# Kernel optimization log

Hardware: AMD Instinct MI355X
Metric: run time of the kernel (lower is better)

The kernel has to match this reference:

```python
import jax, jax.numpy as jnp
import numpy as np
import math

DIM = 1024
N_HEADS = 16
HEAD_DIM = DIM // N_HEADS
FFN_HIDDEN = 4096
EPS = 1e-6


def setup_inputs() -> dict:
    key = jax.random.key(0)
    ks = jax.random.split(key, 10)
    s = 1.0 / math.sqrt(DIM)
    sh = 1.0 / math.sqrt(FFN_HIDDEN)
    return {
        "x": jax.random.normal(ks[0], (2, 2048, DIM), dtype=jnp.float32),
        # attention weights stored as [in, out] (y = x @ W)
        "wq": jax.random.normal(ks[1], (DIM, DIM), dtype=jnp.float32) * s,
        "wk": jax.random.normal(ks[2], (DIM, DIM), dtype=jnp.float32) * s,
        "wv": jax.random.normal(ks[3], (DIM, DIM), dtype=jnp.float32) * s,
        "wo": jax.random.normal(ks[4], (DIM, DIM), dtype=jnp.float32) * s,
        "w_gate": jax.random.normal(ks[5], (DIM, FFN_HIDDEN), dtype=jnp.float32) * s,
        "w_up": jax.random.normal(ks[6], (DIM, FFN_HIDDEN), dtype=jnp.float32) * s,
        "w_down": jax.random.normal(ks[7], (FFN_HIDDEN, DIM), dtype=jnp.float32) * sh,
        "attn_norm_w": jnp.ones((DIM,), dtype=jnp.float32),
        "ffn_norm_w": jnp.ones((DIM,), dtype=jnp.float32),
    }


def rmsnorm(x, w):
    xf = x.astype(jnp.float32)
    rms = jax.lax.rsqrt(jnp.mean(xf * xf, axis=-1, keepdims=True) + EPS)
    return (xf * rms).astype(x.dtype) * w


def attention(x, wq, wk, wv, wo):
    B, T, C = x.shape
    q = (x @ wq).reshape(B, T, N_HEADS, HEAD_DIM)
    k = (x @ wk).reshape(B, T, N_HEADS, HEAD_DIM)
    v = (x @ wv).reshape(B, T, N_HEADS, HEAD_DIM)
    scores = jnp.einsum("bqhd,bkhd->bhqk", q, k) / math.sqrt(HEAD_DIM)
    causal = jnp.tril(jnp.ones((T, T), dtype=bool))  # True = keep
    scores = jnp.where(causal, scores, -jnp.inf)
    attn = jax.nn.softmax(scores, axis=-1)
    out = jnp.einsum("bhqk,bkhd->bqhd", attn, v).reshape(B, T, C)
    return out @ wo


def swiglu(x, w_gate, w_up, w_down):
    return (jax.nn.silu(x @ w_gate) * (x @ w_up)) @ w_down


def reference(x, wq, wk, wv, wo, w_gate, w_up, w_down, attn_norm_w, ffn_norm_w):
    x = x + attention(rmsnorm(x, attn_norm_w), wq, wk, wv, wo)
    x = x + swiglu(rmsnorm(x, ffn_norm_w), w_gate, w_up, w_down)
    return x
```

## Files before the change

kernel.cpp:

```cpp
#include <hip/hip_runtime.h>
#include <hip/hip_bf16.h>
#include <stdint.h>
#include <math.h>

#define DIM   1024
#define TSEQ  2048
#define BATCH 2
#define NH    16
#define HD    64
#define FFN   4096
#define ROWS  (BATCH*TSEQ)
#define QKVN  (3*DIM)

typedef __attribute__((ext_vector_type(8))) short s16x8;
typedef __attribute__((ext_vector_type(4))) float f32x4;

__device__ __forceinline__ unsigned short f2bf(float f) {
  union { float f; unsigned u; } v; v.f = f;
  unsigned r = v.u + 0x7fffu + ((v.u >> 16) & 1u);
  return (unsigned short)(r >> 16);
}
__device__ __forceinline__ float bf2f(unsigned short h) {
  union { unsigned u; float f; } v; v.u = ((unsigned)h) << 16; return v.f;
}
__device__ __forceinline__ unsigned pack_bf2(float lo, float hi) {
  union { float f; unsigned u; } a, c; a.f = lo; c.f = hi;
  return (c.u & 0xffff0000u) | (a.u >> 16);
}

__device__ __forceinline__ void gld16(const void* g, void* l) {
  __builtin_amdgcn_global_load_lds((const __attribute__((address_space(1))) void*)g,
                                   (__attribute__((address_space(3))) void*)l, 16, 0, 0);
}

__device__ __forceinline__ int xcd_swz_flat() {
  const int nx = gridDim.x, ny = gridDim.y;
  const int nwg = nx * ny * gridDim.z;
  const int flat = blockIdx.x + nx * (blockIdx.y + ny * blockIdx.z);
  return (flat & 7) * (nwg >> 3) + (flat >> 3);
}

__global__ void wtrans_k(const float* __restrict__ w, unsigned short* __restrict__ wt,
                         int K, int N, int mode)
{
  __shared__ unsigned short t[64][65];
  const int n0 = blockIdx.x * 64, k0 = blockIdx.y * 64;
  const int tid = threadIdx.x;
  #pragma unroll
  for (int i = 0; i < 16; ++i) {
    const int r = i*4 + (tid >> 6), c = tid & 63;
    t[r][c] = f2bf(w[(size_t)(k0 + r) * N + n0 + c]);
  }
  __syncthreads();
  #pragma unroll
  for (int i = 0; i < 16; ++i) {
    const int r = i*4 + (tid >> 6), c = tid & 63;
    const int n = n0 + r;
    int dr = n;
    if (mode == 1) dr = ((n >> 4) << 5) + (n & 15);
    if (mode == 2) dr = ((n >> 4) << 5) + 16 + (n & 15);
    wt[(size_t)dr * K + k0 + c] = t[c][r];
  }
}

__global__ void wtrans_qkv_k(const float* __restrict__ wq, const float* __restrict__ wk,
                             const float* __restrict__ wv, unsigned short* __restrict__ wt)
{
  __shared__ unsigned short t[64][65];
  const int n0 = blockIdx.x * 64, k0 = blockIdx.y * 64, z = blockIdx.z;
  const float* w = (z == 0) ? wq : (z == 1) ? wk : wv;
  unsigned short* dst = wt + (size_t)z * DIM * DIM;
  const int tid = threadIdx.x;
  #pragma unroll
  for (int i = 0; i < 16; ++i) {
    const int r = i*4 + (tid >> 6), c = tid & 63;
    t[r][c] = f2bf(w[(size_t)(k0 + r) * DIM + n0 + c]);
  }
  __syncthreads();
  #pragma unroll
  for (int i = 0; i < 16; ++i) {
    const int r = i*4 + (tid >> 6), c = tid & 63;
    dst[(size_t)(n0 + r) * DIM + k0 + c] = t[c][r];
  }
}

__global__ void vtrans_k(const unsigned short* __restrict__ qkv, unsigned short* __restrict__ vt)
{
  __shared__ unsigned short t[64][65];
  const int tt0 = blockIdx.x * 64;
  const int bh = blockIdx.y, b = bh >> 4, h = bh & 15;
  const int tid = threadIdx.x;
  const unsigned short* src = qkv + (size_t)(b*TSEQ + tt0) * QKVN + 2*DIM + h*HD;
  #pragma unroll
  for (int i = 0; i < 16; ++i) {
    const int r = i*4 + (tid >> 6), c = tid & 63;
    t[r][c] = src[(size_t)r * QKVN + c];
  }
  __syncthreads();
  unsigned short* dst = vt + (size_t)bh * HD * TSEQ + tt0;
  #pragma unroll
  for (int i = 0; i < 16; ++i) {
    const int d = i*4 + (tid >> 6), c = tid & 63;
    dst[(size_t)d * TSEQ + c] = t[c][d];
  }
}

__global__ void rmsnorm_k(const float* __restrict__ x, const float* __restrict__ w,
                          unsigned short* __restrict__ o)
{
  const int row = blockIdx.x, tid = threadIdx.x;
  const float4 v = ((const float4*)(x + (size_t)row * DIM))[tid];
  float ss = v.x*v.x + v.y*v.y + v.z*v.z + v.w*v.w;
  #pragma unroll
  for (int off = 32; off >= 1; off >>= 1) ss += __shfl_xor(ss, off);
  __shared__ float sred[4];
  if ((tid & 63) == 0) sred[tid >> 6] = ss;
  __syncthreads();
  const float tot = sred[0] + sred[1] + sred[2] + sred[3];
  const float r = rsqrtf(tot * (1.0f/DIM) + 1e-6f);
  const float4 wv = ((const float4*)w)[tid];
  ushort4 ov;
  ov.x = f2bf(v.x*r*wv.x); ov.y = f2bf(v.y*r*wv.y);
  ov.z = f2bf(v.z*r*wv.z); ov.w = f2bf(v.w*r*wv.w);
  ((ushort4*)(o + (size_t)row * DIM))[tid] = ov;
}

__global__ void rmsnorm3_k(const float* __restrict__ x, const float* __restrict__ p0,
                           const float* __restrict__ p1, const float* __restrict__ w,
                           float* __restrict__ x1, unsigned short* __restrict__ o)
{
  const int row = blockIdx.x, tid = threadIdx.x;
  const size_t base = (size_t)row * DIM;
  const float4 a = ((const float4*)(x + base))[tid];
  const float4 b = ((const float4*)(p0 + base))[tid];
  const float4 c = ((const float4*)(p1 + base))[tid];
  float4 v;
  v.x = a.x + b.x + c.x; v.y = a.y + b.y + c.y;
  v.z = a.z + b.z + c.z; v.w = a.w + b.w + c.w;
  ((float4*)(x1 + base))[tid] = v;
  float ss = v.x*v.x + v.y*v.y + v.z*v.z + v.w*v.w;
  #pragma unroll
  for (int off = 32; off >= 1; off >>= 1) ss += __shfl_xor(ss, off);
  __shared__ float sred[4];
  if ((tid & 63) == 0) sred[tid >> 6] = ss;
  __syncthreads();
  const float tot = sred[0] + sred[1] + sred[2] + sred[3];
  const float r = rsqrtf(tot * (1.0f/DIM) + 1e-6f);
  const float4 wv = ((const float4*)w)[tid];
  ushort4 ov;
  ov.x = f2bf(v.x*r*wv.x); ov.y = f2bf(v.y*r*wv.y);
  ov.z = f2bf(v.z*r*wv.z); ov.w = f2bf(v.w*r*wv.w);
  ((ushort4*)(o + base))[tid] = ov;
}

__global__ void resadd3_k(const float* __restrict__ x1, const float* __restrict__ q0,
                          const float* __restrict__ q1, float* __restrict__ o)
{
  const size_t i = (size_t)blockIdx.x * 256 + threadIdx.x;
  const float4 a = ((const float4*)x1)[i];
  const float4 b = ((const float4*)q0)[i];
  const float4 c = ((const float4*)q1)[i];
  float4 v;
  v.x = a.x + b.x + c.x; v.y = a.y + b.y + c.y;
  v.z = a.z + b.z + c.z; v.w = a.w + b.w + c.w;
  ((float4*)o)[i] = v;
}

__global__ void gemm128sp(const unsigned short* __restrict__ A, int lda,
                          const unsigned short* __restrict__ BT, int ldb,
                          float* __restrict__ P, int ldc, int Khalf)
{
  __shared__ __align__(16) unsigned short lA[128*64];
  __shared__ __align__(16) unsigned short lB[128*64];
  const int nx = gridDim.x, ny = gridDim.y;
  const int w = xcd_swz_flat();
  const int bx = w % nx, by = (w / nx) % ny, bz = w / (nx * ny);
  const int tid = threadIdx.x;
  const int lane = tid & 63;
  const int wid = tid >> 6;
  const int m0 = by * 128, n0 = bx * 128;
  const int Koff = bz * Khalf;
  P += (size_t)bz * ((size_t)ny * 128) * ldc;
  const int wr = (wid >> 1) * 64, wc = (wid & 1) * 64;
  const int lrow = lane & 15, lk8 = (lane >> 4) * 8;

  f32x4 acc[4][4] = {};

  for (int k0 = Koff; k0 < Koff + Khalf; k0 += 64) {
    #pragma unroll
    for (int c = 0; c < 4; ++c) {
      const int boff = c*4096 + tid*16;
      const int row = boff >> 7, colb = boff & 127;
      gld16((const char*)A + ((size_t)(m0+row)*lda + k0)*2 + colb, (char*)lA + boff);
    }
    #pragma unroll
    for (int c = 0; c < 4; ++c) {
      const int boff = c*4096 + tid*16;
      const int row = boff >> 7, colb = boff & 127;
      gld16((const char*)BT + ((size_t)(n0+row)*ldb + k0)*2 + colb, (char*)lB + boff);
    }
    __syncthreads();
    #pragma unroll
    for (int kk = 0; kk < 64; kk += 32) {
      s16x8 af[4], bf[4];
      #pragma unroll
      for (int i = 0; i < 4; ++i) af[i] = *(const s16x8*)&lA[(wr + i*16 + lrow)*64 + kk + lk8];
      #pragma unroll
      for (int j = 0; j < 4; ++j) bf[j] = *(const s16x8*)&lB[(wc + j*16 + lrow)*64 + kk + lk8];
      #pragma unroll
      for (int i = 0; i < 4; ++i)
        #pragma unroll
        for (int j = 0; j < 4; ++j)
          acc[i][j] = __builtin_amdgcn_mfma_f32_16x16x32_bf16(af[i], bf[j], acc[i][j], 0, 0, 0);
    }
    __syncthreads();
  }
  const int er = (lane >> 4) * 4, ec = lane & 15;
  #pragma unroll
  for (int i = 0; i < 4; ++i)
    #pragma unroll
    for (int j = 0; j < 4; ++j) {
      const int gr = m0 + wr + i*16 + er;
      const int gc = n0 + wc + j*16 + ec;
      #pragma unroll
      for (int e = 0; e < 4; ++e)
        P[(size_t)(gr + e) * ldc + gc] = acc[i][j][e];
    }
}

template<int EPI>
__global__ __launch_bounds__(512) void gemm256(const unsigned short* __restrict__ A, int lda,
                                               const unsigned short* __restrict__ BT, int ldb,
                                               void* __restrict__ Cout, int ldc, int K)
{
  __shared__ __align__(16) unsigned short lA[2][256*64];
  __shared__ __align__(16) unsigned short lB[2][256*64];
  const int nx = gridDim.x;
  const int wsz = xcd_swz_flat();
  const int bx = wsz % nx, by = wsz / nx;
  const int tid = threadIdx.x, lane = tid & 63, wid = tid >> 6;
  const int lrow = lane & 15, g = lane >> 4;
  const int wm = wid >> 2, wn = wid & 3;
  const int m0 = by * 256, n0 = bx * 256;

  const int r0 = tid >> 3;
  const int eB = ((r0 >> 5) << 6) | (r0 & 31);
  const int lc0 = ((tid & 7) * 16) ^ ((r0 & 7) << 4);
  const char* pA = (const char*)A + ((size_t)(m0 + r0) * lda) * 2 + lc0;
  const char* pB = (const char*)BT + ((size_t)(n0 + eB) * ldb) * 2 + lc0;
  char* dA = (char*)&lA[0][0] + tid * 16;
  char* dB = (char*)&lB[0][0] + eB * 128 + (tid & 7) * 16;
  const size_t a64 = (size_t)64 * lda * 2;
  const size_t b32 = (size_t)32 * ldb * 2;

#define STG_GA0(t) do { const char* s_ = pA + (size_t)(t) * 128; \
    char* d_ = dA + (((t) & 1) * 32768); \
    gld16(s_, d_); gld16(s_ + 2*a64, d_ + 16384); } while (0)
#define STG_GA1(t) do { const char* s_ = pA + (size_t)(t) * 128 + a64; \
    char* d_ = dA + (((t) & 1) * 32768) + 8192; \
    gld16(s_, d_); gld16(s_ + 2*a64, d_ + 16384); } while (0)
#define STG_GB0(t) do { const char* s_ = pB + (size_t)(t) * 128; \
    char* d_ = dB + (((t) & 1) * 32768); \
    gld16(s_, d_); gld16(s_ + 4*b32, d_ + 16384); } while (0)
#define STG_GB1(t) do { const char* s_ = pB + (size_t)(t) * 128 + b32; \
    char* d_ = dB + (((t) & 1) * 32768) + 4096; \
    gld16(s_, d_); gld16(s_ + 4*b32, d_ + 16384); } while (0)

  const int swz = (lrow & 7) << 4;
  const int c0 = (g * 16) ^ swz;
  const int c1 = c0 ^ 64;
  const char* rdA = (const char*)&lA[0][0] + (wm * 128 + lrow) * 128;
  const char* rdB = (const char*)&lB[0][0] + (wn * 64 + lrow) * 128;

  f32x4 acc[8][4] = {};
  s16x8 a0[4][2], a1[4][2], b0[2][2], b1[2][2];

#define MFMA_Q(rh, ch, AF, BF) do { \
    _Pragma("unroll") \
    for (int i_ = 0; i_ < 4; ++i_) { \
      _Pragma("unroll") \
      for (int j_ = 0; j_ < 2; ++j_) { \
        acc[(rh)*4+i_][(ch)*2+j_] = __builtin_amdgcn_mfma_f32_16x16x32_bf16(AF[i_][0], BF[j_][0], acc[(rh)*4+i_][(ch)*2+j_], 0,0,0); \
        acc[(rh)*4+i_][(ch)*2+j_] = __builtin_amdgcn_mfma_f32_16x16x32_bf16(AF[i_][1], BF[j_][1], acc[(rh)*4+i_][(ch)*2+j_], 0,0,0); \
      } } } while (0)

#define VMCNT(n) asm volatile("s_waitcnt vmcnt(" #n ")" ::: "memory")
#define LGKM0()  do { asm volatile("s_waitcnt lgkmcnt(0)" ::: "memory"); \
                      __builtin_amdgcn_sched_barrier(0); } while (0)
#define BARRIER() do { __builtin_amdgcn_s_barrier(); \
                       __builtin_amdgcn_sched_barrier(0); } while (0)

#define DS_A0(buf) do { _Pragma("unroll") for (int i_ = 0; i_ < 4; ++i_) { \
    a0[i_][0] = *(const s16x8*)((buf) + i_*2048 + c0); \
    a0[i_][1] = *(const s16x8*)((buf) + i_*2048 + c1); } } while (0)
#define DS_A1(buf) do { _Pragma("unroll") for (int i_ = 0; i_ < 4; ++i_) { \
    a1[i_][0] = *(const s16x8*)((buf) + 8192 + i_*2048 + c0); \
    a1[i_][1] = *(const s16x8*)((buf) + 8192 + i_*2048 + c1); } } while (0)
#define DS_B0(buf) do { _Pragma("unroll") for (int j_ = 0; j_ < 2; ++j_) { \
    b0[j_][0] = *(const s16x8*)((buf) + j_*2048 + c0); \
    b0[j_][1] = *(const s16x8*)((buf) + j_*2048 + c1); } } while (0)
#define DS_B1(buf) do { _Pragma("unroll") for (int j_ = 0; j_ < 2; ++j_) { \
    b1[j_][0] = *(const s16x8*)((buf) + 4096 + j_*2048 + c0); \
    b1[j_][1] = *(const s16x8*)((buf) + 4096 + j_*2048 + c1); } } while (0)

#define PRIO_MFMA(rh, ch, AF, BF) do { \
    __builtin_amdgcn_s_setprio(1); MFMA_Q(rh, ch, AF, BF); \
    __builtin_amdgcn_s_setprio(0); } while (0)

  const int NT = K >> 6;

  STG_GA0(0); STG_GB0(0); STG_GB1(0); STG_GA1(0);
  VMCNT(4);
  BARRIER();

  for (int t = 0; t < NT - 1; ++t) {
    const char* bufA = rdA + (t & 1) * 32768;
    const char* bufB = rdB + (t & 1) * 32768;
    STG_GA0(t + 1); STG_GB0(t + 1);
    DS_A0(bufA); DS_B0(bufB);
    LGKM0();
    PRIO_MFMA(0, 0, a0, b0);
    VMCNT(6); BARRIER();
    STG_GB1(t + 1);
    DS_B1(bufB);
    LGKM0();
    PRIO_MFMA(0, 1, a0, b1);
    VMCNT(6); BARRIER();
    STG_GA1(t + 1);
    DS_A1(bufA);
    LGKM0();
    PRIO_MFMA(1, 1, a1, b1);
    BARRIER();
    PRIO_MFMA(1, 0, a1, b0);
    VMCNT(4); BARRIER();
  }
  {
    const char* bufA = rdA + ((NT - 1) & 1) * 32768;
    const char* bufB = rdB + ((NT - 1) & 1) * 32768;
    DS_A0(bufA); DS_B0(bufB);
    LGKM0();
    PRIO_MFMA(0, 0, a0, b0);
    VMCNT(2); BARRIER();
    DS_B1(bufB);
    LGKM0();
    PRIO_MFMA(0, 1, a0, b1);
    VMCNT(0); BARRIER();
    DS_A1(bufA);
    LGKM0();
    PRIO_MFMA(1, 1, a1, b1);
    PRIO_MFMA(1, 0, a1, b0);
  }

  const int er = g * 4, ec = lane & 15;
  if (EPI == 0) {
    unsigned short* C = (unsigned short*)Cout;
    #pragma unroll
    for (int i = 0; i < 8; ++i)
      #pragma unroll
      for (int j = 0; j < 4; ++j) {
        const int gr = m0 + wm*128 + i*16 + er;
        const int gc = n0 + wn*64 + j*16 + ec;
        #pragma unroll
        for (int e = 0; e < 4; ++e)
          C[(size_t)(gr + e) * ldc + gc] = f2bf(acc[i][j][e]);
      }
  } else {
    unsigned short* C = (unsigned short*)Cout;
    #pragma unroll
    for (int i = 0; i < 8; ++i)
      #pragma unroll
      for (int tp = 0; tp < 2; ++tp) {
        const int gr = m0 + wm*128 + i*16 + er;
        const int hc = (n0 >> 1) + wn*32 + tp*16 + ec;
        #pragma unroll
        for (int e = 0; e < 4; ++e) {
          const float gv = acc[i][2*tp][e];
          const float uv = acc[i][2*tp + 1][e];
          const float hv = gv / (1.f + __expf(-gv)) * uv;
          C[(size_t)(gr + e) * ldc + hc] = f2bf(hv);
        }
      }
  }
#undef STG_GA0
#undef STG_GA1
#undef STG_GB0
#undef STG_GB1
#undef MFMA_Q
#undef VMCNT
#undef LGKM0
#undef BARRIER
#undef DS_A0
#undef DS_A1
#undef DS_B0
#undef DS_B1
#undef PRIO_MFMA
}

__global__ __launch_bounds__(512) void attn_fwd(const unsigned short* __restrict__ qkv,
                                                const unsigned short* __restrict__ vt,
                                                unsigned short* __restrict__ outp)
{
  __shared__ __align__(16) unsigned short lK[2][64*64];
  __shared__ __align__(16) unsigned short lV[2][64*64];
  const int nx = gridDim.x;
  const int wsz = xcd_swz_flat();
  const int qblk = wsz % nx;
  const int bh = wsz / nx, b = bh >> 4, h = bh & 15;
  const int tid = threadIdx.x, wid = tid >> 6, lane = tid & 63;
  const int lq = lane & 15, g = lane >> 4;

  const int qrow = qblk*128 + wid*16;
  const int myq = qrow + lq;

  const size_t qbase = ((size_t)(b*TSEQ + myq)) * QKVN + h*HD;
  const s16x8 qf0 = *(const s16x8*)&qkv[qbase + g*8];
  const s16x8 qf1 = *(const s16x8*)&qkv[qbase + 32 + g*8];

  const int boff = tid * 16;
  const int loff = boff ^ (((boff >> 7) & 7) << 4);
  const int srow = loff >> 7;
  const int scolb = loff & 127;
  const char* ksrc0 = (const char*)qkv +
      (((size_t)(b*TSEQ + srow)) * QKVN + DIM + h*HD) * 2 + scolb;
  const char* vsrc0 = (const char*)vt +
      (((size_t)bh*HD + srow) * TSEQ) * 2 + scolb;

  float mrun = -INFINITY, lrun = 0.f;
  f32x4 of[4] = {};

  const int nkt = 2*qblk + 2;

  gld16(ksrc0, (char*)lK[0] + boff);
  gld16(vsrc0, (char*)lV[0] + boff);
  int cur = 0;

  for (int kt = 0; kt < nkt; ++kt) {
    __syncthreads();
    if (kt + 1 < nkt) {
      gld16(ksrc0 + (size_t)(kt+1)*64*(QKVN*2), (char*)lK[cur^1] + boff);
      gld16(vsrc0 + (size_t)(kt+1)*128,         (char*)lV[cur^1] + boff);
    }
    if (kt*64 <= qrow + 15) {
      const unsigned short* Kb = lK[cur];
      const unsigned short* Vb = lV[cur];
      f32x4 sacc[4] = {};
      #pragma unroll
      for (int s = 0; s < 4; ++s) {
        const int r = s*16 + lq;
        const int sw = (r & 7) << 4;
        const s16x8 kf0 = *(const s16x8*)((const char*)Kb + r*128 + ((g*16) ^ sw));
        const s16x8 kf1 = *(const s16x8*)((const char*)Kb + r*128 + ((64 + g*16) ^ sw));
        sacc[s] = __builtin_amdgcn_mfma_f32_16x16x32_bf16(kf0, qf0, sacc[s], 0,0,0);
        sacc[s] = __builtin_amdgcn_mfma_f32_16x16x32_bf16(kf1, qf1, sacc[s], 0,0,0);
      }
      float p[4][4];
      float mt = -INFINITY;
      #pragma unroll
      for (int s = 0; s < 4; ++s)
        #pragma unroll
        for (int e = 0; e < 4; ++e) {
          const int key = kt*64 + s*16 + 4*g + e;
          const float v = (key <= myq) ? sacc[s][e]*0.125f : -INFINITY;
          p[s][e] = v;
          mt = fmaxf(mt, v);
        }
      mt = fmaxf(mt, __shfl_xor(mt, 16));
      mt = fmaxf(mt, __shfl_xor(mt, 32));
      const float mnew = fmaxf(mrun, mt);
      const float scale = __expf(mrun - mnew);
      float ssum = 0.f;
      #pragma unroll
      for (int s = 0; s < 4; ++s)
        #pragma unroll
        for (int e = 0; e < 4; ++e) {
          p[s][e] = __expf(p[s][e] - mnew);
          ssum += p[s][e];
        }
      ssum += __shfl_xor(ssum, 16);
      ssum += __shfl_xor(ssum, 32);
      lrun = lrun * scale + ssum;
      mrun = mnew;
      #pragma unroll
      for (int d0b = 0; d0b < 4; ++d0b) of[d0b] = of[d0b] * scale;
      #pragma unroll
      for (int hh = 0; hh < 2; ++hh) {
        unsigned w[4];
        #pragma unroll
        for (int j = 0; j < 4; ++j) w[j] = pack_bf2(p[2*hh][j], p[2*hh+1][j]);
        s16x8 bp;
        #pragma unroll
        for (int e = 0; e < 8; ++e) {
          const int srcg = 2*(g & 1) + (e >> 2);
          const unsigned ww = (unsigned)__shfl((int)w[e & 3], lq | (srcg << 4));
          bp[e] = (short)((g >= 2) ? (ww >> 16) : (ww & 0xffffu));
        }
        #pragma unroll
        for (int d0b = 0; d0b < 4; ++d0b) {
          const int r = d0b*16 + lq;
          const int sw = (r & 7) << 4;
          const s16x8 vf = *(const s16x8*)((const char*)Vb + r*128 + ((hh*64 + g*16) ^ sw));
          of[d0b] = __builtin_amdgcn_mfma_f32_16x16x32_bf16(vf, bp, of[d0b], 0,0,0);
        }
      }
    }
    cur ^= 1;
  }
  const float inv = 1.f / lrun;
  const size_t obase = ((size_t)(b*TSEQ + myq)) * DIM + h*HD;
  #pragma unroll
  for (int d0b = 0; d0b < 4; ++d0b) {
    ushort4 o;
    o.x = f2bf(of[d0b][0] * inv);
    o.y = f2bf(of[d0b][1] * inv);
    o.z = f2bf(of[d0b][2] * inv);
    o.w = f2bf(of[d0b][3] * inv);
    *(ushort4*)&outp[obase + d0b*16 + 4*g] = o;
  }
}

extern "C" void kernel_launch(void* const* d_in, const int* in_sizes, int n_in,
                              void* d_out, int out_size, void* d_ws, size_t ws_size,
                              hipStream_t stream)
{
  const float* x   = (const float*)d_in[0];
  const float* wq  = (const float*)d_in[1];
  const float* wk  = (const float*)d_in[2];
  const float* wv  = (const float*)d_in[3];
  const float* wo  = (const float*)d_in[4];
  const float* wg  = (const float*)d_in[5];
  const float* wu  = (const float*)d_in[6];
  const float* wd  = (const float*)d_in[7];
  const float* anw = (const float*)d_in[8];
  const float* fnw = (const float*)d_in[9];
  float* outp = (float*)d_out;

  const size_t MB = 1024*1024;
  char* ws = (char*)d_ws;
  float*          x1    = (float*)         (ws + 0);
  unsigned short* wdT   = (unsigned short*)(ws + 16*MB);
  unsigned short* wguT  = (unsigned short*)(ws + 24*MB);
  unsigned short* wqkvT = (unsigned short*)(ws + 40*MB);
  unsigned short* woT   = (unsigned short*)(ws + 46*MB);
  unsigned short* xn    = (unsigned short*)(ws + 48*MB);
  unsigned short* qkv   = (unsigned short*)(ws + 56*MB);
  unsigned short* vtb   = (unsigned short*)(ws + 80*MB);
  unsigned short* aout  = (unsigned short*)(ws + 88*MB);
  float*          pwo   = (float*)         (ws + 56*MB);
  unsigned short* hbuf  = (unsigned short*)(ws + 56*MB);
  float*          pdn   = (float*)         (ws + 24*MB);

  const dim3 blk(256);

  wtrans_qkv_k<<<dim3(16,16,3), blk, 0, stream>>>(wq, wk, wv, wqkvT);
  wtrans_k<<<dim3(16,16), blk, 0, stream>>>(wo, woT, DIM, DIM, 0);
  wtrans_k<<<dim3(64,16), blk, 0, stream>>>(wg, wguT, DIM, FFN, 1);
  wtrans_k<<<dim3(64,16), blk, 0, stream>>>(wu, wguT, DIM, FFN, 2);
  wtrans_k<<<dim3(16,64), blk, 0, stream>>>(wd, wdT, FFN, DIM, 0);

  rmsnorm_k<<<ROWS, blk, 0, stream>>>(x, anw, xn);
  gemm256<0><<<dim3(QKVN/256, ROWS/256), dim3(512), 0, stream>>>(xn, DIM, wqkvT, DIM, qkv, QKVN, DIM);
  vtrans_k<<<dim3(TSEQ/64, BATCH*NH), blk, 0, stream>>>(qkv, vtb);
  attn_fwd<<<dim3(TSEQ/128, BATCH*NH), dim3(512), 0, stream>>>(qkv, vtb, aout);
  gemm128sp<<<dim3(DIM/128, ROWS/128, 2), blk, 0, stream>>>(aout, DIM, woT, DIM, pwo, DIM, DIM/2);
  rmsnorm3_k<<<ROWS, blk, 0, stream>>>(x, pwo, pwo + (size_t)ROWS*DIM, fnw, x1, xn);

  gemm256<2><<<dim3(2*FFN/256, ROWS/256), dim3(512), 0, stream>>>(xn, DIM, wguT, DIM, hbuf, FFN, DIM);
  gemm128sp<<<dim3(DIM/128, ROWS/128, 2), blk, 0, stream>>>(hbuf, FFN, wdT, FFN, pdn, DIM, FFN/2);
  resadd3_k<<<dim3(ROWS*DIM/1024), blk, 0, stream>>>(x1, pdn, pdn + (size_t)ROWS*DIM, outp);
}
```

Before: 347.6 us.

## Deepen gemm256 prefetch pipeline, XCD-tiled block mapping, bf16 split-K partials, 4-way down-proj split

Restructures the gemm256 main loop so global loads for the next tile are issued earlier, with register reads for the next stage overlapping the current MFMA quarter. It also replaces the generic XCD swizzle with a CX×CY region mapping meant to improve L2 locality per XCD. Split-K partials in gemm128sp are now stored as bf16 instead of fp32, which halves partial traffic at some cost in precision. The down projection is split 4 ways to raise parallelism, with a 5-input residual add to combine the partials.

```diff
diff --git a/kernel.cpp b/kernel.cpp
--- a/kernel.cpp
+++ b/kernel.cpp
@@ -125,18 +125,18 @@
   ((ushort4*)(o + (size_t)row * DIM))[tid] = ov;
 }
 
-__global__ void rmsnorm3_k(const float* __restrict__ x, const float* __restrict__ p0,
-                           const float* __restrict__ p1, const float* __restrict__ w,
+__global__ void rmsnorm3_k(const float* __restrict__ x, const unsigned short* __restrict__ p0,
+                           const unsigned short* __restrict__ p1, const float* __restrict__ w,
                            float* __restrict__ x1, unsigned short* __restrict__ o)
 {
   const int row = blockIdx.x, tid = threadIdx.x;
   const size_t base = (size_t)row * DIM;
   const float4 a = ((const float4*)(x + base))[tid];
-  const float4 b = ((const float4*)(p0 + base))[tid];
-  const float4 c = ((const float4*)(p1 + base))[tid];
+  const ushort4 b = ((const ushort4*)(p0 + base))[tid];
+  const ushort4 c = ((const ushort4*)(p1 + base))[tid];
   float4 v;
-  v.x = a.x + b.x + c.x; v.y = a.y + b.y + c.y;
-  v.z = a.z + b.z + c.z; v.w = a.w + b.w + c.w;
+  v.x = a.x + bf2f(b.x) + bf2f(c.x); v.y = a.y + bf2f(b.y) + bf2f(c.y);
+  v.z = a.z + bf2f(b.z) + bf2f(c.z); v.w = a.w + bf2f(b.w) + bf2f(c.w);
   ((float4*)(x1 + base))[tid] = v;
   float ss = v.x*v.x + v.y*v.y + v.z*v.z + v.w*v.w;
   #pragma unroll
@@ -153,22 +153,29 @@
   ((ushort4*)(o + base))[tid] = ov;
 }
 
-__global__ void resadd3_k(const float* __restrict__ x1, const float* __restrict__ q0,
-                          const float* __restrict__ q1, float* __restrict__ o)
+__global__ void resadd5_k(const float* __restrict__ x1,
+                          const unsigned short* __restrict__ q0, const unsigned short* __restrict__ q1,
+                          const unsigned short* __restrict__ q2, const unsigned short* __restrict__ q3,
+                          float* __restrict__ o)
 {
   const size_t i = (size_t)blockIdx.x * 256 + threadIdx.x;
   const float4 a = ((const float4*)x1)[i];
-  const float4 b = ((const float4*)q0)[i];
-  const float4 c = ((const float4*)q1)[i];
+  const ushort4 b = ((const ushort4*)q0)[i];
+  const ushort4 c = ((const ushort4*)q1)[i];
+  const ushort4 d = ((const ushort4*)q2)[i];
+  const ushort4 e = ((const ushort4*)q3)[i];
   float4 v;
-  v.x = a.x + b.x + c.x; v.y = a.y + b.y + c.y;
-  v.z = a.z + b.z + c.z; v.w = a.w + b.w + c.w;
+  v.x = a.x + bf2f(b.x) + bf2f(c.x) + bf2f(d.x) + bf2f(e.x);
+  v.y = a.y + bf2f(b.y) + bf2f(c.y) + bf2f(d.y) + bf2f(e.y);
+  v.z = a.z + bf2f(b.z) + bf2f(c.z) + bf2f(d.z) + bf2f(e.z);
+  v.w = a.w + bf2f(b.w) + bf2f(c.w) + bf2f(d.w) + bf2f(e.w);
   ((float4*)o)[i] = v;
 }
 
+template<int NS>
 __global__ void gemm128sp(const unsigned short* __restrict__ A, int lda,
                           const unsigned short* __restrict__ BT, int ldb,
-                          float* __restrict__ P, int ldc, int Khalf)
+                          unsigned short* __restrict__ P, int ldc, int Ksp)
 {
   __shared__ __align__(16) unsigned short lA[128*64];
   __shared__ __align__(16) unsigned short lB[128*64];
@@ -179,14 +186,14 @@
   const int lane = tid & 63;
   const int wid = tid >> 6;
   const int m0 = by * 128, n0 = bx * 128;
-  const int Koff = bz * Khalf;
+  const int Koff = bz * Ksp;
   P += (size_t)bz * ((size_t)ny * 128) * ldc;
   const int wr = (wid >> 1) * 64, wc = (wid & 1) * 64;
   const int lrow = lane & 15, lk8 = (lane >> 4) * 8;
 
   f32x4 acc[4][4] = {};
 
-  for (int k0 = Koff; k0 < Koff + Khalf; k0 += 64) {
+  for (int k0 = Koff; k0 < Koff + Ksp; k0 += 64) {
     #pragma unroll
     for (int c = 0; c < 4; ++c) {
       const int boff = c*4096 + tid*16;
@@ -224,20 +231,25 @@
       const int gc = n0 + wc + j*16 + ec;
       #pragma unroll
       for (int e = 0; e < 4; ++e)
-        P[(size_t)(gr + e) * ldc + gc] = acc[i][j][e];
+        P[(size_t)(gr + e) * ldc + gc] = f2bf(acc[i][j][e]);
     }
 }
 
 template<int EPI>
 __global__ __launch_bounds__(512) void gemm256(const unsigned short* __restrict__ A, int lda,
                                                const unsigned short* __restrict__ BT, int ldb,
-                                               void* __restrict__ Cout, int ldc, int K)
+                                               void* __restrict__ Cout, int ldc, int K,
+                                               int CX, int CY)
 {
   __shared__ __align__(16) unsigned short lA[2][256*64];
   __shared__ __align__(16) unsigned short lB[2][256*64];
-  const int nx = gridDim.x;
-  const int wsz = xcd_swz_flat();
-  const int bx = wsz % nx, by = wsz / nx;
+  const int nx = gridDim.x, ny = gridDim.y;
+  const int flat = blockIdx.x + nx * blockIdx.y;
+  const int xcd = flat & 7, kk_ = flat >> 3;
+  const int RX = nx / CX, RY = ny / CY;
+  const int cx = xcd % CX, cy = xcd / CX;
+  const int bx = cx * RX + kk_ % RX;
+  const int by = cy * RY + kk_ / RX;
   const int tid = threadIdx.x, lane = tid & 63, wid = tid >> 6;
   const int lrow = lane & 15, g = lane >> 4;
   const int wm = wid >> 2, wn = wid & 3;
@@ -290,16 +302,16 @@
 #define BARRIER() do { __builtin_amdgcn_s_barrier(); \
                        __builtin_amdgcn_sched_barrier(0); } while (0)
 
-#define DS_A0(buf) do { _Pragma("unroll") for (int i_ = 0; i_ < 4; ++i_) { \
+#define RD_A0(buf) do { _Pragma("unroll") for (int i_ = 0; i_ < 4; ++i_) { \
     a0[i_][0] = *(const s16x8*)((buf) + i_*2048 + c0); \
     a0[i_][1] = *(const s16x8*)((buf) + i_*2048 + c1); } } while (0)
-#define DS_A1(buf) do { _Pragma("unroll") for (int i_ = 0; i_ < 4; ++i_) { \
+#define RD_A1(buf) do { _Pragma("unroll") for (int i_ = 0; i_ < 4; ++i_) { \
     a1[i_][0] = *(const s16x8*)((buf) + 8192 + i_*2048 + c0); \
     a1[i_][1] = *(const s16x8*)((buf) + 8192 + i_*2048 + c1); } } while (0)
-#define DS_B0(buf) do { _Pragma("unroll") for (int j_ = 0; j_ < 2; ++j_) { \
+#define RD_B0(buf) do { _Pragma("unroll") for (int j_ = 0; j_ < 2; ++j_) { \
     b0[j_][0] = *(const s16x8*)((buf) + j_*2048 + c0); \
     b0[j_][1] = *(const s16x8*)((buf) + j_*2048 + c1); } } while (0)
-#define DS_B1(buf) do { _Pragma("unroll") for (int j_ = 0; j_ < 2; ++j_) { \
+#define RD_B1(buf) do { _Pragma("unroll") for (int j_ = 0; j_ < 2; ++j_) { \
     b1[j_][0] = *(const s16x8*)((buf) + 4096 + j_*2048 + c0); \
     b1[j_][1] = *(const s16x8*)((buf) + 4096 + j_*2048 + c1); } } while (0)
 
@@ -309,46 +321,66 @@
 
   const int NT = K >> 6;
 
-  STG_GA0(0); STG_GB0(0); STG_GB1(0); STG_GA1(0);
-  VMCNT(4);
+  STG_GA0(0); STG_GB0(0); STG_GB1(0); STG_GA1(0); STG_GA0(1); STG_GB0(1);
+  VMCNT(6);
   BARRIER();
-
-  for (int t = 0; t < NT - 1; ++t) {
-    const char* bufA = rdA + (t & 1) * 32768;
-    const char* bufB = rdB + (t & 1) * 32768;
-    STG_GA0(t + 1); STG_GB0(t + 1);
-    DS_A0(bufA); DS_B0(bufB);
-    LGKM0();
+  RD_A0(rdA); RD_B0(rdB);
+
+  for (int t = 0; t < NT - 2; ++t) {
+    const char* Ac = rdA + (t & 1) * 32768;
+    const char* Bc = rdB + (t & 1) * 32768;
+    const char* An = rdA + ((t & 1) ^ 1) * 32768;
+    const char* Bn = rdB + ((t & 1) ^ 1) * 32768;
+    LGKM0();
+    RD_B1(Bc); STG_GB1(t + 1);
     PRIO_MFMA(0, 0, a0, b0);
     VMCNT(6); BARRIER();
-    STG_GB1(t + 1);
-    DS_B1(bufB);
-    LGKM0();
+    LGKM0();
+    RD_A1(Ac); STG_GA1(t + 1);
     PRIO_MFMA(0, 1, a0, b1);
     VMCNT(6); BARRIER();
-    STG_GA1(t + 1);
-    DS_A1(bufA);
-    LGKM0();
+    LGKM0();
+    RD_A0(An); STG_GA0(t + 2);
+    PRIO_MFMA(1, 0, a1, b0);
+    VMCNT(6); BARRIER();
+    RD_B0(Bn); STG_GB0(t + 2);
     PRIO_MFMA(1, 1, a1, b1);
-    BARRIER();
+    VMCNT(6); BARRIER();
+  }
+  {
+    const char* Ac = rdA;
+    const char* Bc = rdB;
+    const char* An = rdA + 32768;
+    const char* Bn = rdB + 32768;
+    LGKM0();
+    RD_B1(Bc); STG_GB1(NT - 1);
+    PRIO_MFMA(0, 0, a0, b0);
+    VMCNT(6); BARRIER();
+    LGKM0();
+    RD_A1(Ac); STG_GA1(NT - 1);
+    PRIO_MFMA(0, 1, a0, b1);
+    VMCNT(6); BARRIER();
+    LGKM0();
+    RD_A0(An);
     PRIO_MFMA(1, 0, a1, b0);
     VMCNT(4); BARRIER();
+    RD_B0(Bn);
+    PRIO_MFMA(1, 1, a1, b1);
+    VMCNT(2); BARRIER();
   }
   {
-    const char* bufA = rdA + ((NT - 1) & 1) * 32768;
-    const char* bufB = rdB + ((NT - 1) & 1) * 32768;
-    DS_A0(bufA); DS_B0(bufB);
-    LGKM0();
+    const char* Ac = rdA + 32768;
+    const char* Bc = rdB + 32768;
+    LGKM0();
+    RD_B1(Bc);
     PRIO_MFMA(0, 0, a0, b0);
-    VMCNT(2); BARRIER();
-    DS_B1(bufB);
-    LGKM0();
+    VMCNT(0); BARRIER();
+    LGKM0();
+    RD_A1(Ac);
     PRIO_MFMA(0, 1, a0, b1);
-    VMCNT(0); BARRIER();
-    DS_A1(bufA);
-    LGKM0();
+    LGKM0();
+    PRIO_MFMA(1, 0, a1, b0);
     PRIO_MFMA(1, 1, a1, b1);
-    PRIO_MFMA(1, 0, a1, b0);
   }
 
   const int er = g * 4, ec = lane & 15;
@@ -389,10 +421,10 @@
 #undef VMCNT
 #undef LGKM0
 #undef BARRIER
-#undef DS_A0
-#undef DS_A1
-#undef DS_B0
-#undef DS_B1
+#undef RD_A0
+#undef RD_A1
+#undef RD_B0
+#undef RD_B1
 #undef PRIO_MFMA
 }
 
@@ -535,6 +567,7 @@
   float* outp = (float*)d_out;
 
   const size_t MB = 1024*1024;
+  const size_t RD = (size_t)ROWS * DIM;
   char* ws = (char*)d_ws;
   float*          x1    = (float*)         (ws + 0);
   unsigned short* wdT   = (unsigned short*)(ws + 16*MB);
@@ -545,9 +578,9 @@
   unsigned short* qkv   = (unsigned short*)(ws + 56*MB);
   unsigned short* vtb   = (unsigned short*)(ws + 80*MB);
   unsigned short* aout  = (unsigned short*)(ws + 88*MB);
-  float*          pwo   = (float*)         (ws + 56*MB);
+  unsigned short* pwo   = (unsigned short*)(ws + 56*MB);
   unsigned short* hbuf  = (unsigned short*)(ws + 56*MB);
-  float*          pdn   = (float*)         (ws + 24*MB);
+  unsigned short* pdn   = (unsigned short*)(ws + 24*MB);
 
   const dim3 blk(256);
 
@@ -558,13 +591,13 @@
   wtrans_k<<<dim3(16,64), blk, 0, stream>>>(wd, wdT, FFN, DIM, 0);
 
   rmsnorm_k<<<ROWS, blk, 0, stream>>>(x, anw, xn);
-  gemm256<0><<<dim3(QKVN/256, ROWS/256), dim3(512), 0, stream>>>(xn, DIM, wqkvT, DIM, qkv, QKVN, DIM);
+  gemm256<0><<<dim3(QKVN/256, ROWS/256), dim3(512), 0, stream>>>(xn, DIM, wqkvT, DIM, qkv, QKVN, DIM, 4, 2);
   vtrans_k<<<dim3(TSEQ/64, BATCH*NH), blk, 0, stream>>>(qkv, vtb);
   attn_fwd<<<dim3(TSEQ/128, BATCH*NH), dim3(512), 0, stream>>>(qkv, vtb, aout);
-  gemm128sp<<<dim3(DIM/128, ROWS/128, 2), blk, 0, stream>>>(aout, DIM, woT, DIM, pwo, DIM, DIM/2);
-  rmsnorm3_k<<<ROWS, blk, 0, stream>>>(x, pwo, pwo + (size_t)ROWS*DIM, fnw, x1, xn);
-
-  gemm256<2><<<dim3(2*FFN/256, ROWS/256), dim3(512), 0, stream>>>(xn, DIM, wguT, DIM, hbuf, FFN, DIM);
-  gemm128sp<<<dim3(DIM/128, ROWS/128, 2), blk, 0, stream>>>(hbuf, FFN, wdT, FFN, pdn, DIM, FFN/2);
-  resadd3_k<<<dim3(ROWS*DIM/1024), blk, 0, stream>>>(x1, pdn, pdn + (size_t)ROWS*DIM, outp);
-}
+  gemm128sp<2><<<dim3(DIM/128, ROWS/128, 2), blk, 0, stream>>>(aout, DIM, woT, DIM, pwo, DIM, DIM/2);
+  rmsnorm3_k<<<ROWS, blk, 0, stream>>>(x, pwo, pwo + RD, fnw, x1, xn);
+
+  gemm256<2><<<dim3(2*FFN/256, ROWS/256), dim3(512), 0, stream>>>(xn, DIM, wguT, DIM, hbuf, FFN, DIM, 4, 2);
+  gemm128sp<4><<<dim3(DIM/128, ROWS/128, 4), blk, 0, stream>>>(hbuf, FFN, wdT, FFN, pdn, DIM, FFN/4);
+  resadd5_k<<<dim3(ROWS*DIM/1024), blk, 0, stream>>>(x1, pdn, pdn + RD, pdn + 2*RD, pdn + 3*RD, outp);
+}
```

After: 298.5 us. -14.1%, faster.
